# Performance work log

Measured on AMD Instinct MI355X. Metric: run time of the kernel, lower is better.

The kernel has to match this reference:

```python
import jax, jax.numpy as jnp
import numpy as np

DIM, H, HD = 512, 8, 64
N_BANK = 4096
EPS = 1e-5


def layernorm(x, g, b):
    m = jnp.mean(x, axis=-1, keepdims=True)
    v = jnp.mean(jnp.square(x - m), axis=-1, keepdims=True)
    return (x - m) * jax.lax.rsqrt(v + EPS) * g + b


def setup_inputs() -> dict:
    key = jax.random.key(0)
    ks = jax.random.split(key, 8)
    # xavier_uniform bound for square (512,512) linears
    bound = float(np.sqrt(6.0 / (DIM + DIM)))
    inp = {
        "x_q": jax.random.normal(ks[0], (32, 128, DIM), jnp.float32),
        "x_k": jax.random.normal(ks[1], (N_BANK, DIM), jnp.float32),
        "x_v": jax.random.normal(ks[2], (N_BANK, DIM), jnp.float32),
        "Wq": jax.random.uniform(ks[3], (DIM, DIM), jnp.float32, -bound, bound),
        "Wk": jax.random.uniform(ks[4], (DIM, DIM), jnp.float32, -bound, bound),
        "Wv": jax.random.uniform(ks[5], (DIM, DIM), jnp.float32, -bound, bound),
        "Wproj": jax.random.uniform(ks[6], (DIM, DIM), jnp.float32, -bound, bound),
        "qn_g": jnp.ones((HD,), jnp.float32),
        "qn_b": jnp.zeros((HD,), jnp.float32),
        "kn_g": jnp.ones((HD,), jnp.float32),
        "kn_b": jnp.zeros((HD,), jnp.float32),
        "n_g": jnp.ones((DIM,), jnp.float32),
        "n_b": jnp.zeros((DIM,), jnp.float32),
    }
    return inp


def reference(x_q, x_k, x_v, Wq, Wk, Wv, Wproj, qn_g, qn_b, kn_g, kn_b, n_g, n_b):
    B, S, D = x_q.shape
    N = x_k.shape[0]
    scale = HD ** (-0.5)
    # Linear layers (torch: y = x @ W.T)
    q = jnp.einsum('bsd,od->bso', x_q, Wq).reshape(B, S, H, HD).transpose(0, 2, 1, 3)  # (B,H,S,hd)
    k = jnp.einsum('nd,od->no', x_k, Wk).reshape(N, H, HD).transpose(1, 0, 2)          # (H,N,hd)
    v = jnp.einsum('nd,od->no', x_v, Wv).reshape(N, H, HD).transpose(1, 0, 2)          # (H,N,hd)
    # per-head qk layernorm
    q = layernorm(q, qn_g, qn_b) * scale
    k = layernorm(k, kn_g, kn_b)
    # cross-attention to shared bank (K/V have no batch dim)
    attn = jnp.einsum('bhsd,hnd->bhsn', q, k)          # (B,H,S,N)
    attn = jax.nn.softmax(attn, axis=-1)
    x = jnp.einsum('bhsn,hnd->bhsd', attn, v)          # (B,H,S,hd)
    x = x.transpose(0, 2, 1, 3).reshape(B, S, D)
    x = layernorm(x, n_g, n_b)
    x = jnp.einsum('bsd,od->bso', x, Wproj)
    return x
```

## Files before the change

### kernel.cpp

```cpp
#include <hip/hip_runtime.h>
#include <hip/hip_bf16.h>
#include <math.h>

#define DIM 512
#define NHEAD 8
#define HD 64
#define NBANK 4096
#define NQROWS 4096
#define EPS 1e-5f
#define QSCALE 0.18033688011f
#define PART_ELEMS (NQROWS * DIM)

typedef __attribute__((ext_vector_type(4))) float floatx4;
typedef __attribute__((ext_vector_type(8))) short short8;

#if defined(__has_builtin)
#if __has_builtin(__builtin_amdgcn_exp2f)
#define EXP2(x) __builtin_amdgcn_exp2f(x)
#endif
#endif
#ifndef EXP2
#define EXP2(x) exp2f(x)
#endif

__device__ __forceinline__ unsigned short f2bf(float f) {
    unsigned int u = __float_as_uint(f);
    u += 0x7fffu + ((u >> 16) & 1u);
    return (unsigned short)(u >> 16);
}
__device__ __forceinline__ float bf2f(unsigned short h) {
    return __uint_as_float(((unsigned int)h) << 16);
}
__device__ __forceinline__ unsigned int pk2(float a, float b) {
    union { __hip_bfloat162 h; unsigned int u; } cvt;
    cvt.h = __float22bfloat162_rn(make_float2(a, b));
    return cvt.u;
}
__device__ __forceinline__ void dma16(const void* gsrc, void* ldst) {
    __builtin_amdgcn_global_load_lds(
        (const __attribute__((address_space(1))) unsigned int*)gsrc,
        (__attribute__((address_space(3))) unsigned int*)ldst, 16, 0, 0);
}

__global__ __launch_bounds__(256) void cvt_kernel(
    const float* __restrict__ Wq, const float* __restrict__ Wk,
    const float* __restrict__ Wv, const float* __restrict__ Wp,
    const float* __restrict__ xq, const float* __restrict__ xk,
    const float* __restrict__ xv,
    unsigned short* __restrict__ Wb, unsigned short* __restrict__ Xb)
{
    const int y = blockIdx.y;
    const float* src;
    unsigned short* dst;
    if (y < 4) {
        if (blockIdx.x >= 128) return;
        src = (y == 0) ? Wq : (y == 1) ? Wk : (y == 2) ? Wv : Wp;
        dst = Wb + (size_t)y * DIM * DIM;
    } else {
        src = (y == 4) ? xq : (y == 5) ? xk : xv;
        dst = Xb + (size_t)(y - 4) * NQROWS * DIM;
    }
    const int i = (blockIdx.x * 256 + threadIdx.x) * 8;
    const int row = i >> 9, kpos = i & 511;
    const int kt = kpos >> 6, seg = (kpos >> 3) & 7;
    const float4 a0 = *(const float4*)(src + i);
    const float4 a1 = *(const float4*)(src + i + 4);
    union { short8 v; unsigned int u[4]; } t;
    t.u[0] = pk2(a0.x, a0.y); t.u[1] = pk2(a0.z, a0.w);
    t.u[2] = pk2(a1.x, a1.y); t.u[3] = pk2(a1.z, a1.w);
    *(short8*)(dst + (size_t)row * 512 + kt * 64 + ((seg ^ (row & 7)) << 3)) = t.v;
}

__global__ __launch_bounds__(256) void qkv_kernel(
    const unsigned short* __restrict__ Xb, const unsigned short* __restrict__ Wb,
    const float* __restrict__ qg, const float* __restrict__ qbeta,
    const float* __restrict__ kg, const float* __restrict__ kbeta,
    unsigned short* __restrict__ Qb, unsigned short* __restrict__ Kb,
    unsigned short* __restrict__ VTb)
{
    __shared__ short8 smem[3072];
    const int tid  = threadIdx.x;
    const int w    = tid >> 6, lane = tid & 63, m = lane & 15, q = lane >> 4;
    const int wr   = w & 1, wc = w >> 1;
    const int row0 = blockIdx.x * 64;
    const int mat  = blockIdx.y >> 2;
    const int col0 = (blockIdx.y & 3) * 128;
    const unsigned short* Xm = Xb + (size_t)mat * NQROWS * DIM;
    const unsigned short* Wm = Wb + (size_t)mat * DIM * DIM;

    const int it0 = tid, it1 = tid + 256;
    const unsigned short* asrc0 = Xm + (size_t)(row0 + (it0 >> 3)) * DIM + (it0 & 7) * 8;
    const unsigned short* asrc1 = Xm + (size_t)(row0 + (it1 >> 3)) * DIM + (it1 & 7) * 8;
    const unsigned short* bsrc[4];
    #pragma unroll
    for (int j = 0; j < 4; ++j) {
        const int item = j * 256 + tid;
        bsrc[j] = Wm + (size_t)(col0 + (item >> 3)) * DIM + (item & 7) * 8;
    }

    floatx4 acc[2][4];
    #pragma unroll
    for (int mt = 0; mt < 2; ++mt)
        #pragma unroll
        for (int nt = 0; nt < 4; ++nt) acc[mt][nt] = (floatx4){0.f, 0.f, 0.f, 0.f};

    {
        short8* as = smem; short8* bs = smem + 512;
        dma16(asrc0, as + w * 64);
        dma16(asrc1, as + 256 + w * 64);
        #pragma unroll
        for (int j = 0; j < 4; ++j)
            dma16(bsrc[j], bs + j * 256 + w * 64);
    }
    __syncthreads();

    for (int kt = 0; kt < 8; ++kt) {
        short8* as = smem + (kt & 1) * 1536;
        short8* bs = as + 512;
        if (kt < 7) {
            short8* asn = smem + ((kt + 1) & 1) * 1536;
            short8* bsn = asn + 512;
            const int o = (kt + 1) * 64;
            dma16(asrc0 + o, asn + w * 64);
            dma16(asrc1 + o, asn + 256 + w * 64);
            #pragma unroll
            for (int j = 0; j < 4; ++j)
                dma16(bsrc[j] + o, bsn + j * 256 + w * 64);
        }
        #pragma unroll
        for (int s = 0; s < 2; ++s) {
            short8 af[2], bfr[4];
            #pragma unroll
            for (int mt = 0; mt < 2; ++mt)
                af[mt] = as[(wr * 32 + mt * 16 + m) * 8 + ((s * 4 + q) ^ (m & 7))];
            #pragma unroll
            for (int nt = 0; nt < 4; ++nt)
                bfr[nt] = bs[(wc * 64 + nt * 16 + m) * 8 + ((s * 4 + q) ^ (m & 7))];
            #pragma unroll
            for (int mt = 0; mt < 2; ++mt)
                #pragma unroll
                for (int nt = 0; nt < 4; ++nt)
                    acc[mt][nt] = __builtin_amdgcn_mfma_f32_16x16x32_bf16(af[mt], bfr[nt], acc[mt][nt], 0, 0, 0);
        }
        __syncthreads();
    }

    if (mat < 2) {
        const float* g = (mat == 0) ? qg : kg;
        const float* be = (mat == 0) ? qbeta : kbeta;
        unsigned short* Y = (mat == 0) ? Qb : Kb;
        float gv[4], bv[4];
        #pragma unroll
        for (int nt = 0; nt < 4; ++nt) { gv[nt] = g[nt * 16 + m]; bv[nt] = be[nt * 16 + m]; }
        #pragma unroll
        for (int mt = 0; mt < 2; ++mt) {
            #pragma unroll
            for (int r = 0; r < 4; ++r) {
                float s = 0.f, sq = 0.f;
                #pragma unroll
                for (int nt = 0; nt < 4; ++nt) { const float v = acc[mt][nt][r]; s += v; sq += v * v; }
                s  += __shfl_xor(s, 1);  s  += __shfl_xor(s, 2);  s  += __shfl_xor(s, 4);  s  += __shfl_xor(s, 8);
                sq += __shfl_xor(sq, 1); sq += __shfl_xor(sq, 2); sq += __shfl_xor(sq, 4); sq += __shfl_xor(sq, 8);
                const float mean = s * (1.f / HD);
                const float var  = sq * (1.f / HD) - mean * mean;
                const float rr   = rsqrtf(var + EPS);
                const int grow = row0 + wr * 32 + mt * 16 + q * 4 + r;
                #pragma unroll
                for (int nt = 0; nt < 4; ++nt) {
                    float v = (acc[mt][nt][r] - mean) * rr * gv[nt] + bv[nt];
                    if (mat == 0) v *= QSCALE;
                    const int col = col0 + wc * 64 + nt * 16 + m;
                    int scol = col;
                    if (mat == 1) {
                        const int o = col & 63, sg2 = o >> 3;
                        scol = (col & ~63) | (((sg2 ^ (grow & 7)) << 3) | (o & 7));
                    }
                    Y[(size_t)grow * DIM + scol] = f2bf(v);
                }
            }
        }
    } else {
        unsigned short* vt = (unsigned short*)smem;
        __syncthreads();
        #pragma unroll
        for (int mt = 0; mt < 2; ++mt)
            #pragma unroll
            for (int nt = 0; nt < 4; ++nt) {
                const int c  = wc * 64 + nt * 16 + m;
                const int rw = wr * 32 + mt * 16 + q * 4;
                *(unsigned int*)(vt + c * 88 + rw)     = pk2(acc[mt][nt][0], acc[mt][nt][1]);
                *(unsigned int*)(vt + c * 88 + rw + 2) = pk2(acc[mt][nt][2], acc[mt][nt][3]);
            }
        __syncthreads();
        #pragma unroll
        for (int p = 0; p < 4; ++p) {
            const int idx = p * 256 + tid;
            const int c = idx >> 3, g = idx & 7;
            const int dglob = col0 + c, hh = dglob >> 6, dl = dglob & 63;
            const int pos = (g >> 2) * 32 + (g & 3) * 4;
            union { short8 v; ushort4 h4[2]; } tv;
            tv.h4[0] = *(const ushort4*)(vt + c * 88 + pos);
            tv.h4[1] = *(const ushort4*)(vt + c * 88 + pos + 16);
            *(short8*)(VTb + ((size_t)(hh * 64 + blockIdx.x) * 512
                              + dl * 8 + (g ^ (dl & 7))) * 8) = tv.v;
        }
    }
}

__global__ __launch_bounds__(256) void attn_kernel(
    const unsigned short* __restrict__ Qb, const unsigned short* __restrict__ Kb,
    const unsigned short* __restrict__ VTb, unsigned short* __restrict__ AOp,
    float* __restrict__ sums)
{
    __shared__ short8 smem[3072];
    const int tid  = threadIdx.x;
    const int w    = tid >> 6;
    const int lane = tid & 63;
    const int m    = lane & 15;
    const int Qd   = lane >> 4;
    const int h    = blockIdx.x & 7;
    const int qgi  = blockIdx.x >> 3;
    const int row0 = qgi * 128;
    const int part = blockIdx.y;
    const int c0   = part * 16;

    const int it0 = tid, it1 = tid + 256;
    const unsigned short* ksrc0 = Kb + (size_t)(it0 >> 3) * DIM + h * HD + (it0 & 7) * 8;
    const unsigned short* ksrc1 = Kb + (size_t)(it1 >> 3) * DIM + h * HD + (it1 & 7) * 8;
    const unsigned short* vbase = VTb + (size_t)h * 64 * 512 * 8;

    short8 qf[2][2];
    #pragma unroll
    for (int mt = 0; mt < 2; ++mt)
        #pragma unroll
        for (int s = 0; s < 2; ++s)
            qf[mt][s] = *(const short8*)(Qb + (size_t)(row0 + w * 32 + mt * 16 + m) * DIM
                                         + h * HD + s * 32 + Qd * 8);

    floatx4 of[4][2];
    float sump[2] = {0.f, 0.f};
    #pragma unroll
    for (int t = 0; t < 4; ++t)
        #pragma unroll
        for (int mt = 0; mt < 2; ++mt) of[t][mt] = (floatx4){0.f, 0.f, 0.f, 0.f};
    const floatx4 fz = (floatx4){0.f, 0.f, 0.f, 0.f};

    {
        short8* ks = smem; short8* vts = smem + 512;
        dma16(ksrc0 + (size_t)c0 * 64 * DIM, ks + w * 64);
        dma16(ksrc1 + (size_t)c0 * 64 * DIM, ks + 256 + w * 64);
        dma16(vbase + ((size_t)c0 * 512 + it0) * 8, vts + w * 64);
        dma16(vbase + ((size_t)c0 * 512 + it1) * 8, vts + 256 + w * 64);
        short8* ks1 = smem + 1024; short8* vts1 = ks1 + 512;
        const size_t c1 = (size_t)c0 + 1;
        dma16(ksrc0 + c1 * 64 * DIM, ks1 + w * 64);
        dma16(ksrc1 + c1 * 64 * DIM, ks1 + 256 + w * 64);
        dma16(vbase + (c1 * 512 + it0) * 8, vts1 + w * 64);
        dma16(vbase + (c1 * 512 + it1) * 8, vts1 + 256 + w * 64);
    }

    int cb = 0, nb = 2;
    for (int c = 0; c < 16; ++c) {
        if (c < 15) asm volatile("s_waitcnt vmcnt(4)" ::: "memory");
        else        asm volatile("s_waitcnt vmcnt(0)" ::: "memory");
        __builtin_amdgcn_s_barrier();
        __builtin_amdgcn_sched_barrier(0);

        short8* ks  = smem + cb * 1024;
        short8* vts = ks + 512;
        if (c < 14) {
            short8* ksn  = smem + nb * 1024;
            short8* vtsn = ksn + 512;
            const size_t nc = (size_t)(c0 + c + 2);
            dma16(ksrc0 + nc * 64 * DIM, ksn + w * 64);
            dma16(ksrc1 + nc * 64 * DIM, ksn + 256 + w * 64);
            dma16(vbase + (nc * 512 + it0) * 8, vtsn + w * 64);
            dma16(vbase + (nc * 512 + it1) * 8, vtsn + 256 + w * 64);
        }

        floatx4 st[4][2];
        #pragma unroll
        for (int t = 0; t < 4; ++t) {
            const short8 kf = ks[(t * 16 + m) * 8 + (Qd ^ (m & 7))];
            #pragma unroll
            for (int mt = 0; mt < 2; ++mt)
                st[t][mt] = __builtin_amdgcn_mfma_f32_16x16x32_bf16(kf, qf[mt][0], fz, 0, 0, 0);
        }
        #pragma unroll
        for (int t = 0; t < 4; ++t) {
            const short8 kf = ks[(t * 16 + m) * 8 + ((4 + Qd) ^ (m & 7))];
            #pragma unroll
            for (int mt = 0; mt < 2; ++mt)
                st[t][mt] = __builtin_amdgcn_mfma_f32_16x16x32_bf16(kf, qf[mt][1], st[t][mt], 0, 0, 0);
        }

        union { short8 v; unsigned int u[4]; } pf[2][2];
        #pragma unroll
        for (int mt = 0; mt < 2; ++mt)
            #pragma unroll
            for (int s2 = 0; s2 < 2; ++s2)
                #pragma unroll
                for (int u = 0; u < 4; ++u) {
                    const int t = s2 * 2 + (u >> 1), r = (u & 1) * 2;
                    const float e0 = EXP2(st[t][mt][r]);
                    const float e1 = EXP2(st[t][mt][r + 1]);
                    sump[mt] += e0;
                    sump[mt] += e1;
                    pf[mt][s2].u[u] = pk2(e0, e1);
                }

        #pragma unroll
        for (int s2 = 0; s2 < 2; ++s2)
            #pragma unroll
            for (int t2 = 0; t2 < 4; ++t2) {
                const short8 vf = vts[(t2 * 16 + m) * 8 + ((s2 * 4 + Qd) ^ (m & 7))];
                #pragma unroll
                for (int mt = 0; mt < 2; ++mt)
                    of[t2][mt] = __builtin_amdgcn_mfma_f32_16x16x32_bf16(vf, pf[mt][s2].v, of[t2][mt], 0, 0, 0);
            }

        cb = (cb == 2) ? 0 : cb + 1;
        nb = (nb == 2) ? 0 : nb + 1;
    }
    __syncthreads();

    #pragma unroll
    for (int mt = 0; mt < 2; ++mt) {
        float s = sump[mt];
        s += __shfl_xor(s, 16);
        s += __shfl_xor(s, 32);
        sump[mt] = s;
    }
    if (Qd == 0) {
        #pragma unroll
        for (int mt = 0; mt < 2; ++mt)
            sums[((size_t)part * NQROWS + row0 + w * 32 + mt * 16 + m) * NHEAD + h] = sump[mt];
    }

    unsigned int* ob = (unsigned int*)smem;
    #pragma unroll
    for (int t2 = 0; t2 < 4; ++t2)
        #pragma unroll
        for (int mt = 0; mt < 2; ++mt) {
            const int qq  = w * 32 + mt * 16 + m;
            const int blk = t2 * 2 + (Qd >> 1);
            const int sub = (Qd & 1) * 2;
            const int bs  = (blk ^ (qq & 7)) * 4;
            ob[qq * 32 + bs + sub]     = pk2(of[t2][mt][0], of[t2][mt][1]);
            ob[qq * 32 + bs + sub + 1] = pk2(of[t2][mt][2], of[t2][mt][3]);
        }
    __syncthreads();
    #pragma unroll
    for (int pp = 0; pp < 4; ++pp) {
        const int idx = tid + pp * 256;
        const int qq = idx >> 3, sg = idx & 7;
        *(short8*)(AOp + (size_t)part * PART_ELEMS + (size_t)(row0 + qq) * DIM + h * HD + sg * 8) =
            smem[qq * 8 + (sg ^ (qq & 7))];
    }
}

__global__ __launch_bounds__(256) void combine_kernel(
    const unsigned short* __restrict__ AOp, const float* __restrict__ sums,
    const float* __restrict__ g, const float* __restrict__ be,
    unsigned short* __restrict__ AO)
{
    __shared__ float rs[256], rq[256], sm[2], sr[2];
    const int tid  = threadIdx.x;
    const int half = tid >> 7;
    const int row  = blockIdx.x * 2 + half;
    const int t    = tid & 127;
    const int h    = t >> 4;

    float stot = 0.f;
    #pragma unroll
    for (int p = 0; p < 4; ++p)
        stot += sums[((size_t)p * NQROWS + row) * NHEAD + h];

    float o[4] = {0.f, 0.f, 0.f, 0.f};
    #pragma unroll
    for (int p = 0; p < 4; ++p) {
        const ushort4 u = *(const ushort4*)(AOp + (size_t)p * PART_ELEMS + (size_t)row * DIM + t * 4);
        o[0] += bf2f(u.x); o[1] += bf2f(u.y); o[2] += bf2f(u.z); o[3] += bf2f(u.w);
    }
    const float inv = 1.0f / stot;
    const float v0 = o[0] * inv, v1 = o[1] * inv, v2 = o[2] * inv, v3 = o[3] * inv;

    rs[tid] = v0 + v1 + v2 + v3;
    rq[tid] = v0 * v0 + v1 * v1 + v2 * v2 + v3 * v3;
    __syncthreads();
    #pragma unroll
    for (int off = 64; off > 0; off >>= 1) {
        if (t < off) { rs[tid] += rs[tid + off]; rq[tid] += rq[tid + off]; }
        __syncthreads();
    }
    if (t == 0) {
        const float mean = rs[tid] * (1.f / DIM);
        const float var  = rq[tid] * (1.f / DIM) - mean * mean;
        sm[half] = mean;
        sr[half] = rsqrtf(var + EPS);
    }
    __syncthreads();

    const float mean = sm[half], rstd = sr[half];
    const float4 g4 = *(const float4*)(g + t * 4);
    const float4 b4 = *(const float4*)(be + t * 4);
    uint2 packed;
    packed.x = pk2((v0 - mean) * rstd * g4.x + b4.x, (v1 - mean) * rstd * g4.y + b4.y);
    packed.y = pk2((v2 - mean) * rstd * g4.z + b4.z, (v3 - mean) * rstd * g4.w + b4.w);
    const int kt = t >> 4, seg = (t >> 1) & 7, jof = (t & 1) * 4;
    *(uint2*)(AO + (size_t)row * DIM + kt * 64 + ((seg ^ (row & 7)) << 3) + jof) = packed;
}

__global__ __launch_bounds__(256) void final_kernel(
    const unsigned short* __restrict__ AO, const unsigned short* __restrict__ Wpb,
    float* __restrict__ out)
{
    __shared__ short8 fs[3072];
    const int tid  = threadIdx.x;
    const int w    = tid >> 6, lane = tid & 63, m = lane & 15, q = lane >> 4;
    const int row0 = blockIdx.x * 64;
    const int col0 = blockIdx.y * 64;

    const int it0 = tid, it1 = tid + 256;
    const unsigned short* asrc0 = AO  + (size_t)(row0 + (it0 >> 3)) * DIM + (it0 & 7) * 8;
    const unsigned short* asrc1 = AO  + (size_t)(row0 + (it1 >> 3)) * DIM + (it1 & 7) * 8;
    const unsigned short* wsrc0 = Wpb + (size_t)(col0 + (it0 >> 3)) * DIM + (it0 & 7) * 8;
    const unsigned short* wsrc1 = Wpb + (size_t)(col0 + (it1 >> 3)) * DIM + (it1 & 7) * 8;

    floatx4 acc[4];
    #pragma unroll
    for (int mt = 0; mt < 4; ++mt) acc[mt] = (floatx4){0.f, 0.f, 0.f, 0.f};

    {
        dma16(asrc0, fs + w * 64);
        dma16(asrc1, fs + 256 + w * 64);
        dma16(wsrc0, fs + 512 + w * 64);
        dma16(wsrc1, fs + 768 + w * 64);
        dma16(asrc0 + 64, fs + 1024 + w * 64);
        dma16(asrc1 + 64, fs + 1024 + 256 + w * 64);
        dma16(wsrc0 + 64, fs + 1024 + 512 + w * 64);
        dma16(wsrc1 + 64, fs + 1024 + 768 + w * 64);
    }

    int cb = 0, nb = 2;
    for (int kt = 0; kt < 8; ++kt) {
        if (kt < 7) asm volatile("s_waitcnt vmcnt(4)" ::: "memory");
        else        asm volatile("s_waitcnt vmcnt(0)" ::: "memory");
        __builtin_amdgcn_s_barrier();
        __builtin_amdgcn_sched_barrier(0);

        short8* buf = fs + cb * 1024;
        if (kt < 6) {
            short8* bufn = fs + nb * 1024;
            const int o = (kt + 2) * 64;
            dma16(asrc0 + o, bufn + w * 64);
            dma16(asrc1 + o, bufn + 256 + w * 64);
            dma16(wsrc0 + o, bufn + 512 + w * 64);
            dma16(wsrc1 + o, bufn + 768 + w * 64);
        }
        #pragma unroll
        for (int s = 0; s < 2; ++s) {
            short8 af[4];
            #pragma unroll
            for (int mt = 0; mt < 4; ++mt)
                af[mt] = buf[(mt * 16 + m) * 8 + ((s * 4 + q) ^ (m & 7))];
            const short8 bfr = buf[512 + (w * 16 + m) * 8 + ((s * 4 + q) ^ (m & 7))];
            #pragma unroll
            for (int mt = 0; mt < 4; ++mt)
                acc[mt] = __builtin_amdgcn_mfma_f32_16x16x32_bf16(af[mt], bfr, acc[mt], 0, 0, 0);
        }
        cb = (cb == 2) ? 0 : cb + 1;
        nb = (nb == 2) ? 0 : nb + 1;
    }

    #pragma unroll
    for (int mt = 0; mt < 4; ++mt)
        #pragma unroll
        for (int r = 0; r < 4; ++r)
            out[(size_t)(row0 + mt * 16 + q * 4 + r) * DIM + col0 + w * 16 + m] = acc[mt][r];
}

extern "C" void kernel_launch(void* const* d_in, const int* in_sizes, int n_in,
                              void* d_out, int out_size, void* d_ws, size_t ws_size,
                              hipStream_t stream)
{
    const float* x_q = (const float*)d_in[0];
    const float* x_k = (const float*)d_in[1];
    const float* x_v = (const float*)d_in[2];
    const float* Wq  = (const float*)d_in[3];
    const float* Wk  = (const float*)d_in[4];
    const float* Wv  = (const float*)d_in[5];
    const float* Wp  = (const float*)d_in[6];
    const float* qg  = (const float*)d_in[7];
    const float* qb  = (const float*)d_in[8];
    const float* kg  = (const float*)d_in[9];
    const float* kb  = (const float*)d_in[10];
    const float* ng  = (const float*)d_in[11];
    const float* nb  = (const float*)d_in[12];
    float* out = (float*)d_out;

    unsigned short* Qb   = (unsigned short*)d_ws;
    unsigned short* Kb   = Qb  + (size_t)NQROWS * DIM;
    unsigned short* VTb  = Kb  + (size_t)NBANK * DIM;
    unsigned short* AOp  = VTb + (size_t)NBANK * DIM;
    float*          sums = (float*)(AOp + (size_t)4 * PART_ELEMS);
    unsigned short* Wb   = (unsigned short*)(sums + (size_t)4 * NQROWS * NHEAD);
    unsigned short* Xb   = AOp;
    unsigned short* AO   = Qb;

    cvt_kernel<<<dim3(1024, 7), 256, 0, stream>>>(Wq, Wk, Wv, Wp, x_q, x_k, x_v, Wb, Xb);
    qkv_kernel<<<dim3(64, 12), 256, 0, stream>>>(Xb, Wb, qg, qb, kg, kb, Qb, Kb, VTb);
    attn_kernel<<<dim3(256, 4), 256, 0, stream>>>(Qb, Kb, VTb, AOp, sums);
    combine_kernel<<<NQROWS / 2, 256, 0, stream>>>(AOp, sums, ng, nb, AO);
    final_kernel<<<dim3(64, 8), 256, 0, stream>>>(AO, Wb + (size_t)3 * DIM * DIM, out);
}
```

Before: 167.2 us.

## Shrink attention LDS ring: triple-buffer K, double-buffer V, target four blocks per CU

The attention kernel's shared-memory pipeline changes from three combined K+V stages (48KB) to three K stages plus two V stages (40KB). V for the next chunk is now issued one iteration ahead instead of two, and the wait counts are adjusted to match. Launch bounds request four blocks per multiprocessor and the chunk loop is fully unrolled. The goal is higher occupancy through a smaller LDS footprint, but the shorter V prefetch distance may expose more load latency and the register cap may cause spills.

```diff
diff --git a/kernel.cpp b/kernel.cpp
--- a/kernel.cpp
+++ b/kernel.cpp
@@ -207,12 +207,12 @@
     }
 }
 
-__global__ __launch_bounds__(256) void attn_kernel(
+__global__ __launch_bounds__(256, 4) void attn_kernel(
     const unsigned short* __restrict__ Qb, const unsigned short* __restrict__ Kb,
     const unsigned short* __restrict__ VTb, unsigned short* __restrict__ AOp,
     float* __restrict__ sums)
 {
-    __shared__ short8 smem[3072];
+    __shared__ short8 smem[2560];
     const int tid  = threadIdx.x;
     const int w    = tid >> 6;
     const int lane = tid & 63;
@@ -246,36 +246,34 @@
     const floatx4 fz = (floatx4){0.f, 0.f, 0.f, 0.f};
 
     {
-        short8* ks = smem; short8* vts = smem + 512;
-        dma16(ksrc0 + (size_t)c0 * 64 * DIM, ks + w * 64);
-        dma16(ksrc1 + (size_t)c0 * 64 * DIM, ks + 256 + w * 64);
-        dma16(vbase + ((size_t)c0 * 512 + it0) * 8, vts + w * 64);
-        dma16(vbase + ((size_t)c0 * 512 + it1) * 8, vts + 256 + w * 64);
-        short8* ks1 = smem + 1024; short8* vts1 = ks1 + 512;
-        const size_t c1 = (size_t)c0 + 1;
-        dma16(ksrc0 + c1 * 64 * DIM, ks1 + w * 64);
-        dma16(ksrc1 + c1 * 64 * DIM, ks1 + 256 + w * 64);
-        dma16(vbase + (c1 * 512 + it0) * 8, vts1 + w * 64);
-        dma16(vbase + (c1 * 512 + it1) * 8, vts1 + 256 + w * 64);
-    }
-
-    int cb = 0, nb = 2;
+        dma16(ksrc0 + (size_t)c0 * 64 * DIM, smem + w * 64);
+        dma16(ksrc1 + (size_t)c0 * 64 * DIM, smem + 256 + w * 64);
+        dma16(vbase + ((size_t)c0 * 512 + it0) * 8, smem + 1536 + w * 64);
+        dma16(vbase + ((size_t)c0 * 512 + it1) * 8, smem + 1536 + 256 + w * 64);
+        dma16(ksrc0 + ((size_t)c0 + 1) * 64 * DIM, smem + 512 + w * 64);
+        dma16(ksrc1 + ((size_t)c0 + 1) * 64 * DIM, smem + 512 + 256 + w * 64);
+    }
+
+    #pragma unroll
     for (int c = 0; c < 16; ++c) {
-        if (c < 15) asm volatile("s_waitcnt vmcnt(4)" ::: "memory");
+        if (c < 15) asm volatile("s_waitcnt vmcnt(2)" ::: "memory");
         else        asm volatile("s_waitcnt vmcnt(0)" ::: "memory");
         __builtin_amdgcn_s_barrier();
         __builtin_amdgcn_sched_barrier(0);
 
-        short8* ks  = smem + cb * 1024;
-        short8* vts = ks + 512;
-        if (c < 14) {
-            short8* ksn  = smem + nb * 1024;
-            short8* vtsn = ksn + 512;
-            const size_t nc = (size_t)(c0 + c + 2);
-            dma16(ksrc0 + nc * 64 * DIM, ksn + w * 64);
-            dma16(ksrc1 + nc * 64 * DIM, ksn + 256 + w * 64);
+        short8* ks  = smem + (c % 3) * 512;
+        short8* vts = smem + 1536 + (c & 1) * 512;
+        if (c < 15) {
+            short8* vtsn = smem + 1536 + ((c + 1) & 1) * 512;
+            const size_t nc = (size_t)(c0 + c + 1);
             dma16(vbase + (nc * 512 + it0) * 8, vtsn + w * 64);
             dma16(vbase + (nc * 512 + it1) * 8, vtsn + 256 + w * 64);
+        }
+        if (c < 14) {
+            short8* ksn = smem + ((c + 2) % 3) * 512;
+            const size_t nc2 = (size_t)(c0 + c + 2);
+            dma16(ksrc0 + nc2 * 64 * DIM, ksn + w * 64);
+            dma16(ksrc1 + nc2 * 64 * DIM, ksn + 256 + w * 64);
         }
 
         floatx4 st[4][2];
@@ -318,9 +316,6 @@
                 for (int mt = 0; mt < 2; ++mt)
                     of[t2][mt] = __builtin_amdgcn_mfma_f32_16x16x32_bf16(vf, pf[mt][s2].v, of[t2][mt], 0, 0, 0);
             }
-
-        cb = (cb == 2) ? 0 : cb + 1;
-        nb = (nb == 2) ? 0 : nb + 1;
     }
     __syncthreads();
 
```

Result: faster. 160.2 us (-4.2%).
